# Performance work log

Measured on AMD Instinct MI355X. Metric: run time of the kernel, lower is better.

Reference implementation:

```python
import jax, jax.numpy as jnp
import numpy as np

H = 2048        # hidden size
NH = 16         # query heads
NKV = 8         # kv heads
HD = 128        # head dim
I = 8192        # intermediate size
EPS = 1e-6
SPLITS = [4194304, 6291456, 8388608, 12582912, 29360128, 46137344]
TOTAL = 62914560


def setup_inputs() -> dict:
    key = jax.random.key(0)
    k1, k2 = jax.random.split(key)
    B, S = 1, 2048
    hidden_states = jax.random.normal(k1, (B, S, H), dtype=jnp.float32)
    flat_weights = jax.random.normal(k2, (TOTAL,), dtype=jnp.float32) * 0.02
    input_ln_w = jnp.ones((H,), dtype=jnp.float32)
    post_ln_w = jnp.ones((H,), dtype=jnp.float32)
    # RoPE tables (Llama theta=10000)
    inv_freq = 1.0 / (10000.0 ** (np.arange(0, HD, 2, dtype=np.float32) / HD))
    ang = np.arange(S, dtype=np.float32)[:, None] * inv_freq[None, :]   # [S, HD/2]
    emb = np.concatenate([ang, ang], axis=-1)                            # [S, HD]
    cos = jnp.asarray(np.cos(emb), dtype=jnp.float32)
    sin = jnp.asarray(np.sin(emb), dtype=jnp.float32)
    return {"hidden_states": hidden_states, "flat_weights": flat_weights,
            "input_ln_w": input_ln_w, "post_ln_w": post_ln_w, "cos": cos, "sin": sin}


def _rms_norm(x, w):
    var = jnp.mean(x * x, axis=-1, keepdims=True)
    return w * (x * jax.lax.rsqrt(var + EPS))


def _rotate_half(x):
    x1, x2 = jnp.split(x, 2, axis=-1)
    return jnp.concatenate([-x2, x1], axis=-1)


def _apply_rope(q, k, cos, sin):
    # q: [B,NH,S,HD], k: [B,NKV,S,HD]; cos/sin: [S,HD]
    c = cos[None, None, :, :]
    s = sin[None, None, :, :]
    return q * c + _rotate_half(q) * s, k * c + _rotate_half(k) * s


def _decoder_layer(hidden_states, flat_weights, input_ln_w, post_ln_w, cos, sin):
    # Simulates dfloat11_decode output: split flat reconstructed weights
    # (split order in source: q, k, v, o, up, gate, down)
    parts = jnp.split(flat_weights, SPLITS)
    q_w = parts[0].reshape(NH * HD, H)
    k_w = parts[1].reshape(NKV * HD, H)
    v_w = parts[2].reshape(NKV * HD, H)
    o_w = parts[3].reshape(H, NH * HD)
    up_w = parts[4].reshape(I, H)
    gate_w = parts[5].reshape(I, H)
    down_w = parts[6].reshape(H, I)

    B, S, _ = hidden_states.shape
    residual = hidden_states
    x = _rms_norm(hidden_states, input_ln_w)

    q = (x @ q_w.T).reshape(B, S, NH, HD).transpose(0, 2, 1, 3)    # [B,NH,S,HD]
    k = (x @ k_w.T).reshape(B, S, NKV, HD).transpose(0, 2, 1, 3)   # [B,NKV,S,HD]
    v = (x @ v_w.T).reshape(B, S, NKV, HD).transpose(0, 2, 1, 3)
    q, k = _apply_rope(q, k, cos, sin)

    # GQA: repeat kv heads
    rep = NH // NKV
    k = jnp.repeat(k, rep, axis=1)   # [B,NH,S,HD]
    v = jnp.repeat(v, rep, axis=1)

    scores = jnp.einsum("bhqd,bhkd->bhqk", q, k) / jnp.sqrt(jnp.float32(HD))
    causal = jnp.tril(jnp.ones((S, S), dtype=bool))
    scores = jnp.where(causal[None, None], scores, jnp.finfo(scores.dtype).min)
    probs = jax.nn.softmax(scores, axis=-1)
    attn = jnp.einsum("bhqk,bhkd->bhqd", probs, v)                  # [B,NH,S,HD]
    attn = attn.transpose(0, 2, 1, 3).reshape(B, S, NH * HD)
    hidden = residual + attn @ o_w.T

    residual = hidden
    x = _rms_norm(hidden, post_ln_w)
    mlp = (jax.nn.silu(x @ gate_w.T) * (x @ up_w.T)) @ down_w.T
    return residual + mlp


def reference(hidden_states, flat_weights, input_ln_w, post_ln_w, cos, sin):
    return _decoder_layer(hidden_states, flat_weights, input_ln_w, post_ln_w, cos, sin)
```

## Files before the change

kernel.cpp:

```cpp
#include <hip/hip_runtime.h>
#include <type_traits>
#include <cstdint>
#include <cstddef>

typedef __bf16 bf16x8 __attribute__((ext_vector_type(8)));
typedef float  f32x4  __attribute__((ext_vector_type(4)));
typedef unsigned short u16v4 __attribute__((ext_vector_type(4)));
typedef unsigned short u16v8 __attribute__((ext_vector_type(8)));

#define H    2048
#define NH   16
#define NKV  8
#define HD   128
#define II   8192
#define S    2048

__device__ __forceinline__ unsigned short f2bf(float f) {
    union { float f; unsigned u; } v; v.f = f;
    unsigned r = v.u + 0x7fffu + ((v.u >> 16) & 1u);
    return (unsigned short)(r >> 16);
}
__device__ __forceinline__ float bf2f(unsigned short b) {
    union { unsigned u; float f; } v; v.u = ((unsigned)b) << 16;
    return v.f;
}

__device__ __forceinline__ void async16(const unsigned short* g, unsigned short* l) {
    __builtin_amdgcn_global_load_lds(
        (const __attribute__((address_space(1))) void*)g,
        (__attribute__((address_space(3))) void*)l, 16, 0, 0);
}

__global__ __launch_bounds__(256) void w2bf(const float* __restrict__ src,
                                            unsigned short* __restrict__ dst)
{
    const size_t i = (size_t)blockIdx.x * 256 + threadIdx.x;
    float4 a = ((const float4*)src)[2 * i];
    float4 b = ((const float4*)src)[2 * i + 1];
    u16v8 o;
    o[0] = f2bf(a.x); o[1] = f2bf(a.y); o[2] = f2bf(a.z); o[3] = f2bf(a.w);
    o[4] = f2bf(b.x); o[5] = f2bf(b.y); o[6] = f2bf(b.z); o[7] = f2bf(b.w);
    ((u16v8*)dst)[i] = o;
}

__global__ __launch_bounds__(256) void rmsnorm_kernel(
    const float* __restrict__ x, const float* __restrict__ w,
    unsigned short* __restrict__ out)
{
    __shared__ float red[4];
    const int row = blockIdx.x;
    const int tid = threadIdx.x;
    const float* xr = x + (size_t)row * H;
    float4 v0 = ((const float4*)xr)[tid];
    float4 v1 = ((const float4*)xr)[256 + tid];
    float s = v0.x*v0.x + v0.y*v0.y + v0.z*v0.z + v0.w*v0.w
            + v1.x*v1.x + v1.y*v1.y + v1.z*v1.z + v1.w*v1.w;
    #pragma unroll
    for (int o = 1; o < 64; o <<= 1) s += __shfl_xor(s, o);
    if ((tid & 63) == 0) red[tid >> 6] = s;
    __syncthreads();
    float tot = red[0] + red[1] + red[2] + red[3];
    float rinv = rsqrtf(tot * (1.0f / (float)H) + 1e-6f);
    float4 w0 = ((const float4*)w)[tid];
    float4 w1 = ((const float4*)w)[256 + tid];
    u16v4 o0, o1;
    o0[0] = f2bf(v0.x * w0.x * rinv); o0[1] = f2bf(v0.y * w0.y * rinv);
    o0[2] = f2bf(v0.z * w0.z * rinv); o0[3] = f2bf(v0.w * w0.w * rinv);
    o1[0] = f2bf(v1.x * w1.x * rinv); o1[1] = f2bf(v1.y * w1.y * rinv);
    o1[2] = f2bf(v1.z * w1.z * rinv); o1[3] = f2bf(v1.w * w1.w * rinv);
    unsigned short* orow = out + (size_t)row * H;
    *(u16v4*)&orow[tid * 4]        = o0;
    *(u16v4*)&orow[1024 + tid * 4] = o1;
}

template<typename OutT, bool ATOMIC>
__global__ __launch_bounds__(256) void gemm_bf16(
    const unsigned short* __restrict__ A, const unsigned short* __restrict__ B,
    OutT* __restrict__ C, int M, int N, int K, int lda, int kslice)
{
    __shared__ unsigned short As[128 * 32];
    __shared__ unsigned short Bs[128 * 32];
    const int tid  = threadIdx.x;
    const int wave = tid >> 6, lane = tid & 63;
    const int quad = lane >> 4, l16 = lane & 15;
    const int m0 = blockIdx.y * 128, n0 = blockIdx.x * 128;
    const int wm = (wave >> 1) * 64, wn = (wave & 1) * 64;
    const int kbeg = blockIdx.z * kslice, kend = kbeg + kslice;

    const int sr = lane >> 2;
    const int sc = (lane & 3) * 8;
    const unsigned short* Ag0 = A + (size_t)(m0 + wave * 16 + sr) * lda + sc + kbeg;
    const unsigned short* Ag1 = Ag0 + (size_t)64 * lda;
    const unsigned short* Bg0 = B + (size_t)(n0 + wave * 16 + sr) * K + sc + kbeg;
    const unsigned short* Bg1 = Bg0 + (size_t)64 * K;
    unsigned short* Al0 = &As[(wave * 16) * 32];
    unsigned short* Al1 = &As[(64 + wave * 16) * 32];
    unsigned short* Bl0 = &Bs[(wave * 16) * 32];
    unsigned short* Bl1 = &Bs[(64 + wave * 16) * 32];

    f32x4 acc[4][4] = {};

    for (int k0 = 0; k0 < kslice; k0 += 32) {
        async16(Ag0 + k0, Al0);
        async16(Ag1 + k0, Al1);
        async16(Bg0 + k0, Bl0);
        async16(Bg1 + k0, Bl1);
        __syncthreads();

        bf16x8 af[4], bfm[4];
        #pragma unroll
        for (int i = 0; i < 4; i++)
            af[i] = *(const bf16x8*)&As[(wm + i * 16 + l16) * 32 + quad * 8];
        #pragma unroll
        for (int i = 0; i < 4; i++)
            bfm[i] = *(const bf16x8*)&Bs[(wn + i * 16 + l16) * 32 + quad * 8];
        #pragma unroll
        for (int mi = 0; mi < 4; mi++)
            #pragma unroll
            for (int ni = 0; ni < 4; ni++)
                acc[mi][ni] = __builtin_amdgcn_mfma_f32_16x16x32_bf16(
                    af[mi], bfm[ni], acc[mi][ni], 0, 0, 0);
        __syncthreads();
    }

    #pragma unroll
    for (int mi = 0; mi < 4; mi++) {
        #pragma unroll
        for (int r = 0; r < 4; r++) {
            const int m = m0 + wm + mi * 16 + quad * 4 + r;
            const size_t rowoff = (size_t)m * N;
            #pragma unroll
            for (int ni = 0; ni < 4; ni++) {
                const int n = n0 + wn + ni * 16 + l16;
                float v = acc[mi][ni][r];
                if constexpr (ATOMIC) {
                    atomicAdd((float*)&C[rowoff + n], v);
                } else if constexpr (std::is_same<OutT, float>::value) {
                    C[rowoff + n] = v;
                } else {
                    C[rowoff + n] = f2bf(v);
                }
            }
        }
    }
}

__global__ __launch_bounds__(256) void rope_prep(
    const unsigned short* __restrict__ qkv, const float* __restrict__ cosp,
    const float* __restrict__ sinp,
    unsigned short* __restrict__ q_r, unsigned short* __restrict__ k_r)
{
    const int s = blockIdx.x;
    const int tid = threadIdx.x;
    const unsigned short* row = qkv + (size_t)s * 4096;
    #pragma unroll
    for (int j = 0; j < 12; j++) {
        int e = j * 256 + tid;
        int head = e >> 7, hd = e & 127;
        float v = bf2f(row[e]);
        float part = (hd < 64) ? -bf2f(row[e + 64]) : bf2f(row[e - 64]);
        float c  = cosp[s * HD + hd];
        float sn = sinp[s * HD + hd];
        unsigned short ob = f2bf(v * c + part * sn);
        if (head < NH) q_r[((size_t)head * S + s) * HD + hd] = ob;
        else           k_r[((size_t)(head - NH) * S + s) * HD + hd] = ob;
    }
}

__global__ __launch_bounds__(256) void v_trans(
    const unsigned short* __restrict__ qkv, unsigned short* __restrict__ v_t)
{
    __shared__ unsigned short t[128][66];
    const int s0 = blockIdx.x * 64;
    const int kv = blockIdx.y;
    const int tid = threadIdx.x;
    const unsigned short* base = qkv + 3072 + kv * HD;
    #pragma unroll
    for (int i = 0; i < 4; i++) {
        int idx = i * 256 + tid;
        int s_l = idx >> 4;
        int hd8 = (idx & 15) * 8;
        u16v8 v = *(const u16v8*)(base + (size_t)(s0 + s_l) * 4096 + hd8);
        #pragma unroll
        for (int j = 0; j < 8; j++) t[hd8 + j][s_l] = v[j];
    }
    __syncthreads();
    #pragma unroll
    for (int i = 0; i < 8; i++) {
        int idx = i * 256 + tid;
        int hd = idx >> 4;
        int s4 = (idx & 15) * 4;
        u16v4 o;
        o[0] = t[hd][s4]; o[1] = t[hd][s4 + 1]; o[2] = t[hd][s4 + 2]; o[3] = t[hd][s4 + 3];
        *(u16v4*)&v_t[((size_t)kv * HD + hd) * S + s0 + s4] = o;
    }
}

__global__ __launch_bounds__(256) void attn_kernel(
    const unsigned short* __restrict__ q_r, const unsigned short* __restrict__ k_r,
    const unsigned short* __restrict__ v_t, unsigned short* __restrict__ out)
{
    __shared__ unsigned short P[4][16][40];
    const int h = blockIdx.y, kv = h >> 1;
    const int qb0 = blockIdx.x * 64;
    const int tid = threadIdx.x;
    const int wave = tid >> 6, lane = tid & 63, quad = lane >> 4, l16 = lane & 15;
    const int qb = qb0 + wave * 16;
    const unsigned short* Q = q_r + (size_t)h * S * HD;
    const unsigned short* K = k_r + (size_t)kv * S * HD;
    const unsigned short* V = v_t + (size_t)kv * HD * S;

    bf16x8 aq[4];
    #pragma unroll
    for (int t = 0; t < 4; t++)
        aq[t] = *(const bf16x8*)&Q[(size_t)(qb + l16) * HD + t * 32 + quad * 8];

    f32x4 o[8] = {};
    float m_i[4] = { -__builtin_inff(), -__builtin_inff(), -__builtin_inff(), -__builtin_inff() };
    float l_i[4] = {};
    const float SCL = 0.08838834764831845f * 1.4426950408889634f;
    const int nk = (qb0 >> 5) + 2;

    for (int kb = 0; kb < nk; kb++) {
        const int kbase = kb * 32;
        f32x4 s0 = {0.f, 0.f, 0.f, 0.f}, s1 = {0.f, 0.f, 0.f, 0.f};
        #pragma unroll
        for (int t = 0; t < 4; t++) {
            bf16x8 b0 = *(const bf16x8*)&K[(size_t)(kbase + l16) * HD + t * 32 + quad * 8];
            bf16x8 b1 = *(const bf16x8*)&K[(size_t)(kbase + 16 + l16) * HD + t * 32 + quad * 8];
            s0 = __builtin_amdgcn_mfma_f32_16x16x32_bf16(aq[t], b0, s0, 0, 0, 0);
            s1 = __builtin_amdgcn_mfma_f32_16x16x32_bf16(aq[t], b1, s1, 0, 0, 0);
        }
        float alpha[4];
        #pragma unroll
        for (int r = 0; r < 4; r++) {
            const int q = qb + quad * 4 + r;
            float v0 = (kbase + l16      <= q) ? s0[r] * SCL : -__builtin_inff();
            float v1 = (kbase + 16 + l16 <= q) ? s1[r] * SCL : -__builtin_inff();
            float mx = fmaxf(v0, v1);
            #pragma unroll
            for (int d = 1; d < 16; d <<= 1) mx = fmaxf(mx, __shfl_xor(mx, d));
            float nm = fmaxf(m_i[r], mx);
            alpha[r] = exp2f(m_i[r] - nm);
            m_i[r] = nm;
            float p0 = exp2f(v0 - nm);
            float p1 = exp2f(v1 - nm);
            s0[r] = p0; s1[r] = p1;
            float rs = p0 + p1;
            #pragma unroll
            for (int d = 1; d < 16; d <<= 1) rs += __shfl_xor(rs, d);
            l_i[r] = l_i[r] * alpha[r] + rs;
        }
        #pragma unroll
        for (int ni = 0; ni < 8; ni++)
            #pragma unroll
            for (int r = 0; r < 4; r++) o[ni][r] *= alpha[r];
        #pragma unroll
        for (int r = 0; r < 4; r++) {
            P[wave][quad * 4 + r][l16]      = f2bf(s0[r]);
            P[wave][quad * 4 + r][16 + l16] = f2bf(s1[r]);
        }
        asm volatile("s_waitcnt lgkmcnt(0)" ::: "memory");
        bf16x8 ap = *(const bf16x8*)&P[wave][l16][quad * 8];
        #pragma unroll
        for (int ni = 0; ni < 8; ni++) {
            bf16x8 bv = *(const bf16x8*)&V[(size_t)(ni * 16 + l16) * S + kbase + quad * 8];
            o[ni] = __builtin_amdgcn_mfma_f32_16x16x32_bf16(ap, bv, o[ni], 0, 0, 0);
        }
    }
    #pragma unroll
    for (int r = 0; r < 4; r++) {
        const float inv = 1.0f / l_i[r];
        const int qrow = qb + quad * 4 + r;
        #pragma unroll
        for (int ni = 0; ni < 8; ni++)
            out[(size_t)qrow * (NH * HD) + h * HD + ni * 16 + l16] = f2bf(o[ni][r] * inv);
    }
}

__global__ __launch_bounds__(256) void silu_mul(unsigned short* __restrict__ m1)
{
    const size_t i = (size_t)blockIdx.x * 256 + threadIdx.x;
    const size_t e = i * 8;
    const int s = (int)(e >> 13);
    const int c = (int)(e & 8191);
    unsigned short* rowp = m1 + (size_t)s * (2 * II);
    u16v8 u = *(const u16v8*)&rowp[c];
    u16v8 g = *(const u16v8*)&rowp[II + c];
    u16v8 r;
    #pragma unroll
    for (int j = 0; j < 8; j++) {
        float gf = bf2f(g[j]);
        float uf = bf2f(u[j]);
        float sig = 1.0f / (1.0f + exp2f(-gf * 1.4426950408889634f));
        r[j] = f2bf(gf * sig * uf);
    }
    *(u16v8*)&rowp[c] = r;
}

extern "C" void kernel_launch(void* const* d_in, const int* in_sizes, int n_in,
                              void* d_out, int out_size, void* d_ws, size_t ws_size,
                              hipStream_t stream) {
    const float* hs   = (const float*)d_in[0];
    const float* W    = (const float*)d_in[1];
    const float* ln1  = (const float*)d_in[2];
    const float* ln2  = (const float*)d_in[3];
    const float* cosp = (const float*)d_in[4];
    const float* sinp = (const float*)d_in[5];
    float* out = (float*)d_out;
    char* ws = (char*)d_ws;

    unsigned short* Wbuf   = (unsigned short*)(ws + 0);
    unsigned short* x_norm = (unsigned short*)(ws + (64ull  << 20));
    unsigned short* qkv    = (unsigned short*)(ws + (72ull  << 20));
    unsigned short* q_r    = (unsigned short*)(ws + (88ull  << 20));
    unsigned short* k_r    = (unsigned short*)(ws + (96ull  << 20));
    unsigned short* v_t    = (unsigned short*)(ws + (100ull << 20));
    unsigned short* attn_o = (unsigned short*)(ws + (104ull << 20));
    unsigned short* mlp1   = (unsigned short*)(ws + (72ull  << 20));

    w2bf<<<8388608 / 2048, 256, 0, stream>>>(W, Wbuf);
    rmsnorm_kernel<<<S, 256, 0, stream>>>(hs, ln1, x_norm);
    gemm_bf16<unsigned short, false><<<dim3(4096 / 128, S / 128, 1), 256, 0, stream>>>(
        x_norm, Wbuf, qkv, S, 4096, H, H, H);
    rope_prep<<<S, 256, 0, stream>>>(qkv, cosp, sinp, q_r, k_r);
    v_trans<<<dim3(S / 64, NKV), 256, 0, stream>>>(qkv, v_t);
    attn_kernel<<<dim3(S / 64, NH), 256, 0, stream>>>(q_r, k_r, v_t, attn_o);
    w2bf<<<4194304 / 2048, 256, 0, stream>>>(W + 8388608, Wbuf);
    hipMemcpyAsync(out, hs, (size_t)S * H * sizeof(float), hipMemcpyDeviceToDevice, stream);
    gemm_bf16<float, true><<<dim3(H / 128, S / 128, 2), 256, 0, stream>>>(
        attn_o, Wbuf, out, S, H, H, H, H / 2);
    rmsnorm_kernel<<<S, 256, 0, stream>>>(out, ln2, x_norm);
    w2bf<<<33554432 / 2048, 256, 0, stream>>>(W + 12582912, Wbuf);
    gemm_bf16<unsigned short, false><<<dim3((2 * II) / 128, S / 128, 1), 256, 0, stream>>>(
        x_norm, Wbuf, mlp1, S, 2 * II, H, H, H);
    silu_mul<<<(S * II / 8) / 256, 256, 0, stream>>>(mlp1);
    w2bf<<<16777216 / 2048, 256, 0, stream>>>(W + 46137344, Wbuf);
    gemm_bf16<float, true><<<dim3(H / 128, S / 128, 4), 256, 0, stream>>>(
        mlp1, Wbuf, out, S, H, II, 2 * II, II / 4);
}
```

Measured before the change: 1.079 ms.

## Stage K/V tiles in LDS with swizzle and fold row-sum into MFMA

The attention kernel now cooperatively loads each 32-key K tile and V tile into shared memory with async global-to-LDS loads and XOR swizzling, so all four waves share one copy instead of each reading K/V from global memory. V is re-laid out by the transpose kernel into contiguous 32-column tiles to make these loads coalesced. The softmax denominator is computed by a ninth MFMA against a ones column appended to V, which removes the shuffle-reduction for the row sum. Waves whose query rows are fully masked skip compute for a tile. The cost is two block barriers per key tile, extra LDS use, and one extra MFMA per tile.

```diff
diff --git a/kernel.cpp b/kernel.cpp
--- a/kernel.cpp
+++ b/kernel.cpp
@@ -25,7 +25,7 @@
     return v.f;
 }
 
-__device__ __forceinline__ void async16(const unsigned short* g, unsigned short* l) {
+__device__ __forceinline__ void async16(const unsigned short* g, const unsigned short* l) {
     __builtin_amdgcn_global_load_lds(
         (const __attribute__((address_space(1))) void*)g,
         (__attribute__((address_space(3))) void*)l, 16, 0, 0);
@@ -85,7 +85,7 @@
     const int quad = lane >> 4, l16 = lane & 15;
     const int m0 = blockIdx.y * 128, n0 = blockIdx.x * 128;
     const int wm = (wave >> 1) * 64, wn = (wave & 1) * 64;
-    const int kbeg = blockIdx.z * kslice, kend = kbeg + kslice;
+    const int kbeg = blockIdx.z * kslice;
 
     const int sr = lane >> 2;
     const int sc = (lane & 3) * 8;
@@ -188,11 +188,15 @@
     #pragma unroll
     for (int i = 0; i < 8; i++) {
         int idx = i * 256 + tid;
-        int hd = idx >> 4;
-        int s4 = (idx & 15) * 4;
+        int d  = idx >> 4;
+        int rm = idx & 15;
+        int hh = rm >> 3;
+        int s4 = (rm & 7) * 4;
         u16v4 o;
-        o[0] = t[hd][s4]; o[1] = t[hd][s4 + 1]; o[2] = t[hd][s4 + 2]; o[3] = t[hd][s4 + 3];
-        *(u16v4*)&v_t[((size_t)kv * HD + hd) * S + s0 + s4] = o;
+        o[0] = t[d][hh * 32 + s4];     o[1] = t[d][hh * 32 + s4 + 1];
+        o[2] = t[d][hh * 32 + s4 + 2]; o[3] = t[d][hh * 32 + s4 + 3];
+        size_t tile = (size_t)kv * (S / 32) + (s0 >> 5) + hh;
+        *(u16v4*)&v_t[(tile * 128 + d) * 32 + s4] = o;
     }
 }
 
@@ -200,77 +204,104 @@
     const unsigned short* __restrict__ q_r, const unsigned short* __restrict__ k_r,
     const unsigned short* __restrict__ v_t, unsigned short* __restrict__ out)
 {
+    __shared__ unsigned short Ks[32 * 128];
+    __shared__ unsigned short Vs[144 * 32];
     __shared__ unsigned short P[4][16][40];
     const int h = blockIdx.y, kv = h >> 1;
     const int qb0 = blockIdx.x * 64;
     const int tid = threadIdx.x;
     const int wave = tid >> 6, lane = tid & 63, quad = lane >> 4, l16 = lane & 15;
     const int qb = qb0 + wave * 16;
-    const unsigned short* Q = q_r + (size_t)h * S * HD;
-    const unsigned short* K = k_r + (size_t)kv * S * HD;
-    const unsigned short* V = v_t + (size_t)kv * HD * S;
+    const unsigned short* Q  = q_r + (size_t)h * S * HD;
+    const unsigned short* K  = k_r + (size_t)kv * S * HD;
+    const unsigned short* Vh = v_t + (size_t)kv * (S / 32) * (128 * 32);
+
+    {
+        int e0 = tid * 2;
+        Vs[128 * 32 + e0]     = (e0     < 32) ? (unsigned short)0x3F80 : (unsigned short)0;
+        Vs[128 * 32 + e0 + 1] = (e0 + 1 < 32) ? (unsigned short)0x3F80 : (unsigned short)0;
+    }
 
     bf16x8 aq[4];
     #pragma unroll
     for (int t = 0; t < 4; t++)
         aq[t] = *(const bf16x8*)&Q[(size_t)(qb + l16) * HD + t * 32 + quad * 8];
 
-    f32x4 o[8] = {};
+    f32x4 o[9] = {};
     float m_i[4] = { -__builtin_inff(), -__builtin_inff(), -__builtin_inff(), -__builtin_inff() };
-    float l_i[4] = {};
     const float SCL = 0.08838834764831845f * 1.4426950408889634f;
     const int nk = (qb0 >> 5) + 2;
 
+    const int kr  = (lane >> 4);
+    const int kbl = lane & 15;
+    const int vr  = (lane >> 2);
+    const int vbl = lane & 3;
+
     for (int kb = 0; kb < nk; kb++) {
         const int kbase = kb * 32;
-        f32x4 s0 = {0.f, 0.f, 0.f, 0.f}, s1 = {0.f, 0.f, 0.f, 0.f};
-        #pragma unroll
-        for (int t = 0; t < 4; t++) {
-            bf16x8 b0 = *(const bf16x8*)&K[(size_t)(kbase + l16) * HD + t * 32 + quad * 8];
-            bf16x8 b1 = *(const bf16x8*)&K[(size_t)(kbase + 16 + l16) * HD + t * 32 + quad * 8];
-            s0 = __builtin_amdgcn_mfma_f32_16x16x32_bf16(aq[t], b0, s0, 0, 0, 0);
-            s1 = __builtin_amdgcn_mfma_f32_16x16x32_bf16(aq[t], b1, s1, 0, 0, 0);
+        const unsigned short* Ktile = K + (size_t)kbase * HD;
+        const unsigned short* Vtile = Vh + (size_t)kb * (128 * 32);
+        #pragma unroll
+        for (int e = 0; e < 2; e++) {
+            int r = wave * 8 + e * 4 + kr;
+            async16(Ktile + r * 128 + ((kbl ^ (r & 15)) * 8), &Ks[(wave * 8 + e * 4) * 128]);
         }
-        float alpha[4];
-        #pragma unroll
-        for (int r = 0; r < 4; r++) {
-            const int q = qb + quad * 4 + r;
-            float v0 = (kbase + l16      <= q) ? s0[r] * SCL : -__builtin_inff();
-            float v1 = (kbase + 16 + l16 <= q) ? s1[r] * SCL : -__builtin_inff();
-            float mx = fmaxf(v0, v1);
-            #pragma unroll
-            for (int d = 1; d < 16; d <<= 1) mx = fmaxf(mx, __shfl_xor(mx, d));
-            float nm = fmaxf(m_i[r], mx);
-            alpha[r] = exp2f(m_i[r] - nm);
-            m_i[r] = nm;
-            float p0 = exp2f(v0 - nm);
-            float p1 = exp2f(v1 - nm);
-            s0[r] = p0; s1[r] = p1;
-            float rs = p0 + p1;
-            #pragma unroll
-            for (int d = 1; d < 16; d <<= 1) rs += __shfl_xor(rs, d);
-            l_i[r] = l_i[r] * alpha[r] + rs;
+        #pragma unroll
+        for (int e = 0; e < 2; e++) {
+            int d = wave * 32 + e * 16 + vr;
+            async16(Vtile + d * 32 + ((vbl ^ (d & 3)) * 8), &Vs[(wave * 32 + e * 16) * 32]);
         }
-        #pragma unroll
-        for (int ni = 0; ni < 8; ni++)
-            #pragma unroll
-            for (int r = 0; r < 4; r++) o[ni][r] *= alpha[r];
-        #pragma unroll
-        for (int r = 0; r < 4; r++) {
-            P[wave][quad * 4 + r][l16]      = f2bf(s0[r]);
-            P[wave][quad * 4 + r][16 + l16] = f2bf(s1[r]);
+        __syncthreads();
+
+        if (kbase <= qb + 15) {
+            f32x4 s0 = {0.f, 0.f, 0.f, 0.f}, s1 = {0.f, 0.f, 0.f, 0.f};
+            #pragma unroll
+            for (int t = 0; t < 4; t++) {
+                int b = t * 4 + quad;
+                bf16x8 b0 = *(const bf16x8*)&Ks[l16 * 128 + ((b ^ l16) * 8)];
+                bf16x8 b1 = *(const bf16x8*)&Ks[(16 + l16) * 128 + ((b ^ l16) * 8)];
+                s0 = __builtin_amdgcn_mfma_f32_16x16x32_bf16(aq[t], b0, s0, 0, 0, 0);
+                s1 = __builtin_amdgcn_mfma_f32_16x16x32_bf16(aq[t], b1, s1, 0, 0, 0);
+            }
+            float alpha[4];
+            #pragma unroll
+            for (int r = 0; r < 4; r++) {
+                const int q = qb + quad * 4 + r;
+                float v0 = (kbase + l16      <= q) ? s0[r] * SCL : -__builtin_inff();
+                float v1 = (kbase + 16 + l16 <= q) ? s1[r] * SCL : -__builtin_inff();
+                float mx = fmaxf(v0, v1);
+                #pragma unroll
+                for (int d = 1; d < 16; d <<= 1) mx = fmaxf(mx, __shfl_xor(mx, d));
+                float nm = fmaxf(m_i[r], mx);
+                alpha[r] = exp2f(m_i[r] - nm);
+                m_i[r] = nm;
+                s0[r] = exp2f(v0 - nm);
+                s1[r] = exp2f(v1 - nm);
+            }
+            #pragma unroll
+            for (int ni = 0; ni < 9; ni++)
+                #pragma unroll
+                for (int r = 0; r < 4; r++) o[ni][r] *= alpha[r];
+            #pragma unroll
+            for (int r = 0; r < 4; r++) {
+                P[wave][quad * 4 + r][l16]      = f2bf(s0[r]);
+                P[wave][quad * 4 + r][16 + l16] = f2bf(s1[r]);
+            }
+            asm volatile("s_waitcnt lgkmcnt(0)" ::: "memory");
+            bf16x8 ap = *(const bf16x8*)&P[wave][l16][quad * 8];
+            #pragma unroll
+            for (int ni = 0; ni < 9; ni++) {
+                int d = ni * 16 + l16;
+                bf16x8 bv = *(const bf16x8*)&Vs[d * 32 + ((quad ^ (d & 3)) * 8)];
+                o[ni] = __builtin_amdgcn_mfma_f32_16x16x32_bf16(ap, bv, o[ni], 0, 0, 0);
+            }
         }
-        asm volatile("s_waitcnt lgkmcnt(0)" ::: "memory");
-        bf16x8 ap = *(const bf16x8*)&P[wave][l16][quad * 8];
-        #pragma unroll
-        for (int ni = 0; ni < 8; ni++) {
-            bf16x8 bv = *(const bf16x8*)&V[(size_t)(ni * 16 + l16) * S + kbase + quad * 8];
-            o[ni] = __builtin_amdgcn_mfma_f32_16x16x32_bf16(ap, bv, o[ni], 0, 0, 0);
-        }
+        __syncthreads();
     }
     #pragma unroll
     for (int r = 0; r < 4; r++) {
-        const float inv = 1.0f / l_i[r];
+        float lsum = __shfl(o[8][r], quad * 16);
+        const float inv = 1.0f / lsum;
         const int qrow = qb + quad * 4 + r;
         #pragma unroll
         for (int ni = 0; ni < 8; ni++)
```

New measurement: 945.9 us. -12.3%, faster.
